# Kernel tuning notes

Measured on AMD Instinct MI355X. Metric: run time of the kernel, lower is better.

Reference implementation:

```python
import jax, jax.numpy as jnp
import numpy as np

V = 32000
MASK_ID = 31999
EPS = 1e-3          # log-linear schedule eps
DT = 0.05           # reverse-step size
NUCLEUS_P = 0.9
NEG_INF = -1000000.0
B, S = 2, 1024


def move_chance(t):
    # BD3-LM log-linear schedule: move_chance(t) = (1 - eps) * t
    return (1.0 - EPS) * t


def nucleus_filter(probs, p):
    # descending sort over vocab
    order = jnp.argsort(-probs, axis=-1)                     # [B,S,V]
    sorted_probs = jnp.take_along_axis(probs, order, axis=-1)
    cum = jnp.cumsum(sorted_probs, axis=-1)
    keep = cum <= p
    keep = keep.at[..., 0].set(True)                          # always keep top-1
    kept = sorted_probs * keep
    inv = jnp.argsort(order, axis=-1)                         # inverse permutation
    filtered = jnp.take_along_axis(kept, inv, axis=-1)        # scatter back
    return filtered / jnp.sum(filtered, axis=-1, keepdims=True)


def setup_inputs() -> dict:
    key = jax.random.key(0)
    k1, k2, k3, k4 = jax.random.split(key, 4)
    x = jax.random.randint(k1, (B, S), 0, V, dtype=jnp.int32)
    m = jax.random.uniform(k4, (B, S)) < 0.5
    x = jnp.where(m, MASK_ID, x)
    logits = jax.random.normal(k2, (B, S, V), dtype=jnp.float32)
    t = jnp.ones((1,), dtype=jnp.float32)
    u = jax.random.uniform(k3, (B, S, V), dtype=jnp.float32)
    return {"x": x, "logits": logits, "t": t, "u": u}


def reference(x, logits, t, u):
    mct = move_chance(t)[..., None]          # [1,1]
    mcs = move_chance(t - DT)[..., None]     # [1,1]
    mask_prob = mcs / mct                    # [1,1], broadcasts over [S,V]

    logits = logits.at[:, :, MASK_ID].set(NEG_INF)
    p_x0 = jax.nn.softmax(logits, axis=-1)   # [B,S,V]
    p_x0 = nucleus_filter(p_x0, NUCLEUS_P)

    q_xs = p_x0 * (1.0 - mask_prob)
    q_xs = q_xs.at[:, :, MASK_ID].set(jnp.squeeze(mask_prob, -1))

    gumbel = -jnp.log(-jnp.log(u + 1e-10) + 1e-10)
    x_new = jnp.argmax(q_xs / (gumbel + 1e-10), axis=-1).astype(x.dtype)

    is_masked = x == MASK_ID
    x_new = jnp.where(is_masked, x_new, x)
    return x_new, p_x0
```

## Files before the change

kernel.cpp:

```cpp
#include <hip/hip_runtime.h>

#define NVOC 32000
#define NV4  (NVOC / 4)
#define MASKID 31999
#define NBINS 1024
#define NTHR 512
#define NWAVES (NTHR / 64)
#define LISTCAP 2048

typedef unsigned int u32;
typedef unsigned long long u64;

__device__ __forceinline__ int bin_e(float e) {
    int v = (int)(__float_as_uint(e) >> 17) - 6976;
    v = v < 0 ? 0 : v;
    return v > (NBINS - 1) ? (NBINS - 1) : v;
}

__device__ __forceinline__ u32 fix32(float e) {
    float x = e * 4294967296.0f;
    x = fminf(x, 4294967040.0f);
    return (u32)x;
}

__global__ __launch_bounds__(NTHR, 8) void mdlm_kernel(
    const int* __restrict__ xin,
    const float* __restrict__ logits,
    const float* __restrict__ tin,
    const float* __restrict__ uin,
    float* __restrict__ out,
    int rows)
{
    __shared__ u64 sHist[NBINS];
    __shared__ u32 sList[LISTCAP];
    __shared__ float sRedF[NWAVES];
    __shared__ int sRedI[NWAVES];
    __shared__ double sRedD[NWAVES];
    __shared__ float sZmax, sTT;
    __shared__ int sCnt, sB, sCross, sMaxDrop;
    __shared__ u32 sTau;
    __shared__ u64 sAs, sSfp;

    const int row = blockIdx.x;
    if (row >= rows) return;
    const int tid = threadIdx.x;
    const float4* lrow4 = (const float4*)(logits + (size_t)row * NVOC);
    const float4* urow4 = (const float4*)(uin + (size_t)row * NVOC);
    float* prow = out + (size_t)rows + (size_t)row * NVOC;

    sHist[tid] = 0ULL;
    sHist[tid + NTHR] = 0ULL;
    if (tid == 0) {
        sCnt = 0; sB = -1; sCross = 0; sMaxDrop = -1; sTau = 0xFFFFFFFFu;
        sAs = 0ULL; sSfp = 0ULL;
        sTT = tin[0];
    }
    __syncthreads();

    float lmax = -3.0e38f;
    for (int v4 = tid; v4 < NV4; v4 += NTHR) {
        float4 f = lrow4[v4];
        if (v4 == (MASKID >> 2)) f.w = -1000000.0f;
        lmax = fmaxf(lmax, fmaxf(fmaxf(f.x, f.y), fmaxf(f.z, f.w)));
    }
    for (int off = 32; off > 0; off >>= 1)
        lmax = fmaxf(lmax, __shfl_down(lmax, off, 64));
    if ((tid & 63) == 0) sRedF[tid >> 6] = lmax;
    __syncthreads();
    if (tid == 0) {
        float m = sRedF[0];
        for (int w = 1; w < NWAVES; ++w) m = fmaxf(m, sRedF[w]);
        sZmax = m;
    }
    __syncthreads();
    const float zmax = sZmax;

    for (int v4 = tid; v4 < NV4; v4 += NTHR) {
        float4 f = lrow4[v4];
        if (v4 == (MASKID >> 2)) f.w = -1000000.0f;
        float ex = __expf(f.x - zmax);
        float ey = __expf(f.y - zmax);
        float ez = __expf(f.z - zmax);
        float ew = __expf(f.w - zmax);
        atomicAdd(&sHist[bin_e(ex)], (u64)fix32(ex));
        atomicAdd(&sHist[bin_e(ey)], (u64)fix32(ey));
        atomicAdd(&sHist[bin_e(ez)], (u64)fix32(ez));
        atomicAdd(&sHist[bin_e(ew)], (u64)fix32(ew));
    }
    __syncthreads();

    for (int dlt = 1; dlt < NBINS; dlt <<= 1) {
        u64 v0 = (tid + dlt < NBINS) ? sHist[tid + dlt] : 0ULL;
        u64 v1 = (tid + NTHR + dlt < NBINS) ? sHist[tid + NTHR + dlt] : 0ULL;
        __syncthreads();
        sHist[tid] += v0;
        sHist[tid + NTHR] += v1;
        __syncthreads();
    }
    const double T = 0.9 * (double)sHist[0];
    {
#pragma unroll
        for (int h = 0; h < 2; ++h) {
            int b = tid + h * NTHR;
            u64 Ai = sHist[b];
            u64 As = (b + 1 < NBINS) ? sHist[b + 1] : 0ULL;
            bool dropped = ((double)As >= T);
            bool keptf = ((double)Ai <= T);
            if (dropped) atomicMax(&sMaxDrop, b);
            if (!dropped && !keptf) { sB = b; sCross = 1; }
        }
    }
    __syncthreads();
    if (tid == 0) {
        int B = sCross ? sB : sMaxDrop;
        sB = B;
        u64 As;
        if (B < 0) As = sHist[0];
        else As = (B + 1 < NBINS) ? sHist[B + 1] : 0ULL;
        sAs = As;
        if (!sCross) sSfp = As;
    }
    __syncthreads();

    const int Bst = sB;
    const int cross = sCross;

    if (cross) {
        for (int v4 = tid; v4 < NV4; v4 += NTHR) {
            float4 f = lrow4[v4];
            if (v4 == (MASKID >> 2)) f.w = -1000000.0f;
            float ee[4];
            ee[0] = __expf(f.x - zmax);
            ee[1] = __expf(f.y - zmax);
            ee[2] = __expf(f.z - zmax);
            ee[3] = __expf(f.w - zmax);
#pragma unroll
            for (int e4 = 0; e4 < 4; ++e4) {
                if (bin_e(ee[e4]) == Bst) {
                    int pos = atomicAdd(&sCnt, 1);
                    if (pos < LISTCAP) sList[pos] = fix32(ee[e4]);
                }
            }
        }
        __syncthreads();
        const int K = sCnt < LISTCAP ? sCnt : LISTCAP;
        for (int jj = tid; jj < K; jj += NTHR) {
            u32 mj = sList[jj];
            u64 s = sAs;
            for (int q2 = 0; q2 < K; ++q2) {
                u32 mv = sList[q2];
                if (mv >= mj) s += (u64)mv;
            }
            if ((double)s <= T) atomicMin(&sTau, mj);
        }
        __syncthreads();
        if (tid == 0) sSfp = sAs;
        __syncthreads();
        u32 tl = sTau;
        if (tl != 0xFFFFFFFFu) {
            u64 part = 0ULL;
            for (int q2 = tid; q2 < K; q2 += NTHR) {
                u32 mv = sList[q2];
                if (mv >= tl) part += (u64)mv;
            }
            if (part) atomicAdd(&sSfp, part);
        }
        __syncthreads();
    }

    u32 tauU;
    {
        u32 tv = sTau;
        u32 edgefix = 0u;
        if (Bst >= 0) edgefix = fix32(__uint_as_float((u32)(Bst + 1 + 6976) << 17));
        if (cross) tauU = (tv != 0xFFFFFFFFu) ? tv : edgefix;
        else       tauU = (Bst < 0) ? 0u : edgefix;
    }

    const double invSd = 4294967296.0 / (double)sSfp;
    const float invSf = (float)invSd;

    double mpd, omd;
    {
        double td = (double)sTT;
        mpd = ((1.0 - 1e-3) * (td - 0.05)) / ((1.0 - 1e-3) * td);
        omd = 1.0 - mpd;
    }
    const float mqf = (float)(mpd / omd);

    float r1 = -3.0e38f, r2 = -3.0e38f;
    float q1 = 0.0f,     q2 = 0.0f;
    int   i1 = 0,        i2 = 0;
    for (int v4 = tid; v4 < NV4; v4 += NTHR) {
        float4 uf = urow4[v4];
        float4 f = lrow4[v4];
        if (v4 == (MASKID >> 2)) f.w = -1000000.0f;
        float ee[4], uu[4] = {uf.x, uf.y, uf.z, uf.w};
        ee[0] = __expf(f.x - zmax);
        ee[1] = __expf(f.y - zmax);
        ee[2] = __expf(f.z - zmax);
        ee[3] = __expf(f.w - zmax);
        float4 po;
        float pp[4];
        const int i0 = v4 * 4;
#pragma unroll
        for (int e4 = 0; e4 < 4; ++e4) {
            float e = ee[e4];
            float p = (fix32(e) >= tauU) ? e * invSf : 0.0f;
            pp[e4] = p;
            float g = -__logf(1e-10f - __logf(uu[e4] + 1e-10f));
            float r = p * __builtin_amdgcn_rcpf(g + 1e-10f);
            if (r > r1)      { r2 = r1; q2 = q1; i2 = i1; r1 = r; q1 = p; i1 = i0 + e4; }
            else if (r > r2) { r2 = r;  q2 = p;  i2 = i0 + e4; }
        }
        po.x = pp[0]; po.y = pp[1]; po.z = pp[2]; po.w = pp[3];
        ((float4*)prow)[v4] = po;
    }
    if (tid == ((MASKID >> 2) % NTHR)) {
        float um = ((const float*)urow4)[MASKID];
        float g = -__logf(1e-10f - __logf(um + 1e-10f));
        float rm = mqf * __builtin_amdgcn_rcpf(g + 1e-10f);
        if (rm > r1)      { r2 = r1; q2 = q1; i2 = i1; r1 = rm; q1 = 0.0f; i1 = MASKID; }
        else if (rm > r2) { r2 = rm; q2 = 0.0f; i2 = MASKID; }
    }

    double best; int bidx;
    {
        const float* urowf = (const float*)urow4;
        double qa = (i1 == MASKID) ? mpd : (double)q1 * omd;
        double g1 = -log(-log((double)urowf[i1] + 1e-10) + 1e-10);
        best = qa / (g1 + 1e-10);
        bidx = i1;
        double qb = (i2 == MASKID) ? mpd : (double)q2 * omd;
        double g2 = -log(-log((double)urowf[i2] + 1e-10) + 1e-10);
        double rd = qb / (g2 + 1e-10);
        if (rd > best || (rd == best && i2 < bidx)) { best = rd; bidx = i2; }
    }

    for (int off = 32; off > 0; off >>= 1) {
        double ov = __shfl_down(best, off, 64);
        int oi = __shfl_down(bidx, off, 64);
        if (ov > best || (ov == best && oi < bidx)) { best = ov; bidx = oi; }
    }
    if ((tid & 63) == 0) { sRedD[tid >> 6] = best; sRedI[tid >> 6] = bidx; }
    __syncthreads();
    if (tid == 0) {
        best = sRedD[0]; bidx = sRedI[0];
        for (int w = 1; w < NWAVES; ++w) {
            double ov = sRedD[w]; int oi = sRedI[w];
            if (ov > best || (ov == best && oi < bidx)) { best = ov; bidx = oi; }
        }
        int xv = xin[row];
        out[row] = (float)((xv == MASKID) ? bidx : xv);
    }
}

extern "C" void kernel_launch(void* const* d_in, const int* in_sizes, int n_in,
                              void* d_out, int out_size, void* d_ws, size_t ws_size,
                              hipStream_t stream) {
    const int* x = (const int*)d_in[0];
    const float* logits = (const float*)d_in[1];
    const float* t = (const float*)d_in[2];
    const float* u = (const float*)d_in[3];
    float* out = (float*)d_out;
    const int rows = in_sizes[0];
    hipLaunchKernelGGL(mdlm_kernel, dim3(rows), dim3(NTHR), 0, stream,
                       x, logits, t, u, out, rows);
}
```

Baseline: 268.4 us.

## Cache fixed-point exp values in output buffer to avoid recomputing softmax

The histogram pass now writes each element's fixed-point exp value into the output probability row, and the later candidate-list and final sampling passes read those cached integers instead of reloading logits and recomputing exp. Histogram binning is redone on the integer mantissa so bin edges and the threshold are consistent with the cached values. This trades repeated logit reads and exp evaluations for an extra global write plus re-reads of the row, which are likely L2-resident. It also changes the threshold edge computation, which carries some risk to exact tie handling.

```diff
diff --git a/kernel.cpp b/kernel.cpp
--- a/kernel.cpp
+++ b/kernel.cpp
@@ -11,16 +11,17 @@
 typedef unsigned int u32;
 typedef unsigned long long u64;
 
-__device__ __forceinline__ int bin_e(float e) {
-    int v = (int)(__float_as_uint(e) >> 17) - 6976;
-    v = v < 0 ? 0 : v;
-    return v > (NBINS - 1) ? (NBINS - 1) : v;
-}
-
 __device__ __forceinline__ u32 fix32(float e) {
     float x = e * 4294967296.0f;
     x = fminf(x, 4294967040.0f);
     return (u32)x;
+}
+
+__device__ __forceinline__ int bin_m(u32 m) {
+    float fm = (float)m;
+    int v = (int)(__float_as_uint(fm) >> 18) - 4064;
+    v = v < 0 ? 0 : v;
+    return v > (NBINS - 1) ? (NBINS - 1) : v;
 }
 
 __global__ __launch_bounds__(NTHR, 8) void mdlm_kernel(
@@ -47,6 +48,7 @@
     const float4* lrow4 = (const float4*)(logits + (size_t)row * NVOC);
     const float4* urow4 = (const float4*)(uin + (size_t)row * NVOC);
     float* prow = out + (size_t)rows + (size_t)row * NVOC;
+    uint4* mrow4 = (uint4*)prow;
 
     sHist[tid] = 0ULL;
     sHist[tid + NTHR] = 0ULL;
@@ -78,14 +80,16 @@
     for (int v4 = tid; v4 < NV4; v4 += NTHR) {
         float4 f = lrow4[v4];
         if (v4 == (MASKID >> 2)) f.w = -1000000.0f;
-        float ex = __expf(f.x - zmax);
-        float ey = __expf(f.y - zmax);
-        float ez = __expf(f.z - zmax);
-        float ew = __expf(f.w - zmax);
-        atomicAdd(&sHist[bin_e(ex)], (u64)fix32(ex));
-        atomicAdd(&sHist[bin_e(ey)], (u64)fix32(ey));
-        atomicAdd(&sHist[bin_e(ez)], (u64)fix32(ez));
-        atomicAdd(&sHist[bin_e(ew)], (u64)fix32(ew));
+        u32 mx = fix32(__expf(f.x - zmax));
+        u32 my = fix32(__expf(f.y - zmax));
+        u32 mz = fix32(__expf(f.z - zmax));
+        u32 mw = fix32(__expf(f.w - zmax));
+        atomicAdd(&sHist[bin_m(mx)], (u64)mx);
+        atomicAdd(&sHist[bin_m(my)], (u64)my);
+        atomicAdd(&sHist[bin_m(mz)], (u64)mz);
+        atomicAdd(&sHist[bin_m(mw)], (u64)mw);
+        uint4 mo; mo.x = mx; mo.y = my; mo.z = mz; mo.w = mw;
+        mrow4[v4] = mo;
     }
     __syncthreads();
 
@@ -127,18 +131,14 @@
 
     if (cross) {
         for (int v4 = tid; v4 < NV4; v4 += NTHR) {
-            float4 f = lrow4[v4];
-            if (v4 == (MASKID >> 2)) f.w = -1000000.0f;
-            float ee[4];
-            ee[0] = __expf(f.x - zmax);
-            ee[1] = __expf(f.y - zmax);
-            ee[2] = __expf(f.z - zmax);
-            ee[3] = __expf(f.w - zmax);
+            uint4 mv4 = mrow4[v4];
+            u32 mm[4] = {mv4.x, mv4.y, mv4.z, mv4.w};
 #pragma unroll
             for (int e4 = 0; e4 < 4; ++e4) {
-                if (bin_e(ee[e4]) == Bst) {
+                u32 m = mm[e4];
+                if (m && bin_m(m) == Bst) {
                     int pos = atomicAdd(&sCnt, 1);
-                    if (pos < LISTCAP) sList[pos] = fix32(ee[e4]);
+                    if (pos < LISTCAP) sList[pos] = m;
                 }
             }
         }
@@ -171,14 +171,20 @@
     u32 tauU;
     {
         u32 tv = sTau;
-        u32 edgefix = 0u;
-        if (Bst >= 0) edgefix = fix32(__uint_as_float((u32)(Bst + 1 + 6976) << 17));
-        if (cross) tauU = (tv != 0xFFFFFFFFu) ? tv : edgefix;
-        else       tauU = (Bst < 0) ? 0u : edgefix;
-    }
-
-    const double invSd = 4294967296.0 / (double)sSfp;
-    const float invSf = (float)invSd;
+        bool useTau = cross && (tv != 0xFFFFFFFFu);
+        if (useTau) tauU = tv;
+        else if (Bst < 0) tauU = 0u;
+        else if (Bst + 1 >= NBINS) tauU = 0xFFFFFFFFu;
+        else {
+            float fedge = __uint_as_float((u32)(4064 + Bst + 1) << 18);
+            u32 t = (u32)fedge;
+            while (t > 0u && (float)(t - 1u) >= fedge) --t;
+            while ((float)t < fedge) ++t;
+            tauU = t;
+        }
+    }
+
+    const float invSmf = (float)(1.0 / (double)sSfp);
 
     double mpd, omd;
     {
@@ -193,26 +199,22 @@
     int   i1 = 0,        i2 = 0;
     for (int v4 = tid; v4 < NV4; v4 += NTHR) {
         float4 uf = urow4[v4];
-        float4 f = lrow4[v4];
-        if (v4 == (MASKID >> 2)) f.w = -1000000.0f;
-        float ee[4], uu[4] = {uf.x, uf.y, uf.z, uf.w};
-        ee[0] = __expf(f.x - zmax);
-        ee[1] = __expf(f.y - zmax);
-        ee[2] = __expf(f.z - zmax);
-        ee[3] = __expf(f.w - zmax);
-        float4 po;
+        uint4 mv4 = mrow4[v4];
+        u32 mm[4] = {mv4.x, mv4.y, mv4.z, mv4.w};
+        float uu[4] = {uf.x, uf.y, uf.z, uf.w};
         float pp[4];
         const int i0 = v4 * 4;
 #pragma unroll
         for (int e4 = 0; e4 < 4; ++e4) {
-            float e = ee[e4];
-            float p = (fix32(e) >= tauU) ? e * invSf : 0.0f;
+            u32 m = mm[e4];
+            float p = (m >= tauU) ? (float)m * invSmf : 0.0f;
             pp[e4] = p;
             float g = -__logf(1e-10f - __logf(uu[e4] + 1e-10f));
             float r = p * __builtin_amdgcn_rcpf(g + 1e-10f);
             if (r > r1)      { r2 = r1; q2 = q1; i2 = i1; r1 = r; q1 = p; i1 = i0 + e4; }
             else if (r > r2) { r2 = r;  q2 = p;  i2 = i0 + e4; }
         }
+        float4 po;
         po.x = pp[0]; po.y = pp[1]; po.z = pp[2]; po.w = pp[3];
         ((float4*)prow)[v4] = po;
     }
```

After: 317.4 us. 1.18x slower.
